# Kernel tuning notes

Measured on AMD Instinct MI355X. Metric: run time of the kernel, lower is better.

## Reference

```python
import jax, jax.numpy as jnp
import numpy as np

B, S, D = 2, 2048, 2048
H, KV, HD = 32, 8, 64
REP = H // KV


def rotate_half(t):
    t1, t2 = t[..., : t.shape[-1] // 2], t[..., t.shape[-1] // 2 :]
    return jnp.concatenate((-t2, t1), axis=-1)


def setup_inputs() -> dict:
    key = jax.random.key(0)
    kx, kq, kk, kv, ko = jax.random.split(key, 5)
    x = jax.random.normal(kx, (B, S, D), dtype=jnp.float32) * 0.02
    # RoPE tables: shape [S, HD//2]; forward concatenates [cos, cos] to reach HD
    inv_freq = 1.0 / (10000.0 ** (np.arange(0, HD, 2, dtype=np.float32) / HD))
    freqs = np.outer(np.arange(S, dtype=np.float32), inv_freq)
    cos = jnp.asarray(np.cos(freqs), dtype=jnp.float32)
    sin = jnp.asarray(np.sin(freqs), dtype=jnp.float32)
    # causal additive mask [1,1,S,S]
    causal = np.tril(np.ones((S, S), dtype=bool))
    mask = jnp.asarray(np.where(causal, 0.0, -1e9).astype(np.float32))[None, None]
    s = 0.02
    wq = jax.random.normal(kq, (H * HD, D), dtype=jnp.float32) * s
    wk = jax.random.normal(kk, (KV * HD, D), dtype=jnp.float32) * s
    wv = jax.random.normal(kv, (KV * HD, D), dtype=jnp.float32) * s
    wo = jax.random.normal(ko, (D, H * HD), dtype=jnp.float32) * s
    return {"x": x, "cos": cos, "sin": sin, "mask": mask,
            "wq": wq, "wk": wk, "wv": wv, "wo": wo}


def reference(x, cos, sin, mask, wq, wk, wv, wo):
    b, s, d = x.shape
    # QKV projections (Linear with bias=False: x @ W^T)
    q = jnp.einsum("bsd,ed->bse", x, wq).reshape(b, s, H, HD)
    k = jnp.einsum("bsd,ed->bse", x, wk).reshape(b, s, KV, HD)
    v = jnp.einsum("bsd,ed->bse", x, wv).reshape(b, s, KV, HD)
    # RoPE: cos/sin [S, HD//2] -> [1, S, 1, HD]
    cc = jnp.concatenate([cos[:s], cos[:s]], axis=-1)[None, :, None, :]
    ss = jnp.concatenate([sin[:s], sin[:s]], axis=-1)[None, :, None, :]
    q = q * cc + rotate_half(q) * ss
    k = k * cc + rotate_half(k) * ss
    # GQA: group q heads by kv head (implicit broadcast instead of repeat_kv)
    q = q.transpose(0, 2, 1, 3).reshape(b, KV, REP, s, HD)  # [B,KV,REP,S,HD]
    k = k.transpose(0, 2, 1, 3)                              # [B,KV,S,HD]
    v = v.transpose(0, 2, 1, 3)                              # [B,KV,S,HD]
    scores = jnp.einsum("bkrqd,bksd->bkrqs", q, k) / np.sqrt(HD)
    scores = scores + mask[:, :, None, :, :]  # broadcast over rep dim
    probs = jax.nn.softmax(scores.astype(jnp.float32), axis=-1).astype(q.dtype)
    out = jnp.einsum("bkrqs,bksd->bkrqd", probs, v)
    out = out.transpose(0, 3, 1, 2, 4).reshape(b, s, H * HD)  # [B,S,H*HD]
    return jnp.einsum("bse,de->bsd", out, wo)
```

## Files before the change

### kernel.cpp

```cpp
#include <hip/hip_runtime.h>
#include <stdint.h>

#define DEV __device__ __forceinline__

typedef __bf16 bf16;
typedef __bf16 bf16x8 __attribute__((ext_vector_type(8)));
typedef __bf16 bf16x4v __attribute__((ext_vector_type(4)));
typedef float f32x4 __attribute__((ext_vector_type(4)));
typedef float f32x16 __attribute__((ext_vector_type(16)));
typedef int int2v __attribute__((ext_vector_type(2)));

constexpr int Bb = 2, Ss = 2048, Dd = 2048, Hh = 32, KVh = 8, HDd = 64;
constexpr int Mm = Bb * Ss;
constexpr int EQ = Hh * HDd;
constexpr int EKV = KVh * HDd;
constexpr int Ee = EQ + 2 * EKV;

DEV void gload16(const void* g, void* l) {
  __builtin_amdgcn_global_load_lds((const __attribute__((address_space(1))) uint32_t*)g,
                                   (__attribute__((address_space(3))) uint32_t*)l, 16, 0, 0);
}

DEV float exp2_fast(float x) {
  float r;
  asm("v_exp_f32 %0, %1\n\ts_nop 0" : "=v"(r) : "v"(x));
  return r;
}
DEV uint32_t cvtpk(float lo, float hi) {
  uint32_t w;
  asm("v_cvt_pk_bf16_f32 %0, %1, %2" : "=v"(w) : "v"(lo), "v"(hi));
  return w;
}
DEV int2v pswap(uint32_t a, uint32_t b) {
  return __builtin_amdgcn_permlane32_swap((int)a, (int)b, false, false);
}
DEV float fu(uint32_t u) { union { uint32_t u; float f; } c; c.u = u; return c.f; }
DEV uint32_t uf(float f) { union { float f; uint32_t u; } c; c.f = f; return c.u; }

__global__ void cvt_kernel(const float* __restrict__ x, const float* __restrict__ wq,
                           const float* __restrict__ wk, const float* __restrict__ wv,
                           const float* __restrict__ wo,
                           bf16* __restrict__ xb, bf16* __restrict__ wqkvb,
                           bf16* __restrict__ wob) {
  const long NX = (long)Mm * Dd;
  const long NQ = (long)EQ * Dd;
  const long NK = (long)EKV * Dd;
  const long NO = (long)Dd * EQ;
  const long total4 = (NX + NQ + 2 * NK + NO) / 4;
  for (long i = (long)blockIdx.x * blockDim.x + threadIdx.x; i < total4;
       i += (long)gridDim.x * blockDim.x) {
    long e = i * 4;
    const float* src; bf16* dst;
    if (e < NX)                { src = x + e;                       dst = xb + e; }
    else if (e < NX + NQ)      { long o = e - NX;                   src = wq + o; dst = wqkvb + o; }
    else if (e < NX + NQ + NK) { long o = e - NX - NQ;              src = wk + o; dst = wqkvb + NQ + o; }
    else if (e < NX + NQ + 2*NK){ long o = e - NX - NQ - NK;        src = wv + o; dst = wqkvb + NQ + NK + o; }
    else                       { long o = e - NX - NQ - 2*NK;       src = wo + o; dst = wob + o; }
    float4 v = *(const float4*)src;
    bf16x4v b;
    b.x = (bf16)v.x; b.y = (bf16)v.y; b.z = (bf16)v.z; b.w = (bf16)v.w;
    *(bf16x4v*)dst = b;
  }
}

template <int BN, bool OUT_BF16>
__global__ __launch_bounds__(512, 1)
void gemm_bt(const bf16* __restrict__ A, const bf16* __restrict__ Bt,
             float* __restrict__ Cf, bf16* __restrict__ Cb,
             int Mn, int Nn, int Kn) {
  constexpr int NJ = BN / 64;
  constexpr int RB = BN / 4;
  __shared__ __align__(16) bf16 As[2][256 * 64];
  __shared__ __align__(16) bf16 Bs[2][BN * 64];
  const int tid = threadIdx.x, wid = tid >> 6, lane = tid & 63;
  const int g = lane >> 4, c = lane & 15;
  const int wm = wid >> 2, wn = wid & 3;

  const int nbj = Nn / BN;
  const int nwg = (Mn >> 8) * nbj;
  const int cpx = nwg >> 3;
  const int swz = ((int)blockIdx.x % 8) * cpx + (int)blockIdx.x / 8;
  const int bi = swz / nbj, bj = swz % nbj;
  const long arow0 = (long)bi * 256, brow0 = (long)bj * BN;

  const int srow = tid >> 3, schk = tid & 7;
  const int cs = schk ^ (srow & 7);

  f32x4 acc[8][NJ] = {};

#pragma unroll
  for (int it = 0; it < 4; ++it)
    gload16(A + (arow0 + it * 64 + srow) * Kn + cs * 8,
            (char*)&As[0][0] + it * 8192 + tid * 16);
#pragma unroll
  for (int q = 0; q < NJ; ++q)
    gload16(Bt + (brow0 + q * 64 + srow) * Kn + cs * 8,
            (char*)&Bs[0][0] + q * 8192 + tid * 16);
  __syncthreads();

  const int NT = Kn >> 6;
  for (int kt = 0; kt < NT; ++kt) {
    const char* pa = (const char*)&As[kt & 1][0];
    const char* pb = (const char*)&Bs[kt & 1][0];
    char* na = (char*)&As[(kt + 1) & 1][0];
    char* nb = (char*)&Bs[(kt + 1) & 1][0];
    const bool more = (kt + 1 < NT);
    bf16x8 bfr[NJ][2];

#pragma unroll
    for (int p = 0; p < 4; ++p) {
      bf16x8 af[2][2];
#pragma unroll
      for (int i2 = 0; i2 < 2; ++i2)
#pragma unroll
        for (int ks = 0; ks < 2; ++ks) {
          int r = wm * 128 + (2 * p + i2) * 16 + c;
          af[i2][ks] = *(const bf16x8*)(pa + r * 128 + (((ks * 4 + g) ^ (r & 7)) << 4));
        }
      if (p == 0) {
#pragma unroll
        for (int j = 0; j < NJ; ++j)
#pragma unroll
          for (int ks = 0; ks < 2; ++ks) {
            int r = wn * RB + j * 16 + c;
            bfr[j][ks] = *(const bf16x8*)(pb + r * 128 + (((ks * 4 + g) ^ (r & 7)) << 4));
          }
      }
      if (more) {
        if (p < NJ)
          gload16(Bt + (brow0 + p * 64 + srow) * Kn + (kt + 1) * 64 + cs * 8,
                  nb + p * 8192 + tid * 16);
        gload16(A + (arow0 + p * 64 + srow) * Kn + (kt + 1) * 64 + cs * 8,
                na + p * 8192 + tid * 16);
      }
      __builtin_amdgcn_s_barrier();
      asm volatile("s_waitcnt lgkmcnt(0)" ::: "memory");
      __builtin_amdgcn_s_setprio(1);
#pragma unroll
      for (int i2 = 0; i2 < 2; ++i2)
#pragma unroll
        for (int j = 0; j < NJ; ++j)
#pragma unroll
          for (int ks = 0; ks < 2; ++ks)
            acc[2 * p + i2][j] =
                __builtin_amdgcn_mfma_f32_16x16x32_bf16(af[i2][ks], bfr[j][ks],
                                                        acc[2 * p + i2][j], 0, 0, 0);
      __builtin_amdgcn_s_setprio(0);
      if (p == 1) asm volatile("s_waitcnt vmcnt(4)" ::: "memory");
      if (p < 3) __builtin_amdgcn_s_barrier();
    }
    asm volatile("s_waitcnt vmcnt(1)" ::: "memory");
    __builtin_amdgcn_s_barrier();
  }

#pragma unroll
  for (int i = 0; i < 8; ++i)
#pragma unroll
    for (int j = 0; j < NJ; ++j)
#pragma unroll
      for (int r = 0; r < 4; ++r) {
        long row = arow0 + wm * 128 + i * 16 + 4 * g + r;
        long col = brow0 + wn * RB + j * 16 + c;
        if (OUT_BF16) Cb[row * Nn + col] = (bf16)acc[i][j][r];
        else          Cf[row * Nn + col] = acc[i][j][r];
      }
}

__global__ void kv_prep_kernel(const bf16* __restrict__ qkv, const float* __restrict__ cosT,
                               const float* __restrict__ sinT, bf16* __restrict__ kout,
                               bf16* __restrict__ vtb) {
  if (blockIdx.x < 512) {
    __shared__ __align__(16) unsigned short tile[64][72];
    int blk = blockIdx.x;
    int st = blk & 31, kvh = (blk >> 5) & 7, b = blk >> 8;
    int s0 = st * 64;
    int t = threadIdx.x;
#pragma unroll
    for (int rep = 0; rep < 2; ++rep) {
      int idx = t + rep * 256;
      int r = idx >> 3, cb = idx & 7;
      const bf16* src = qkv + ((long)(b * Ss + s0 + r)) * Ee + EQ + EKV + kvh * 64 + cb * 8;
      *(uint4*)&tile[r][cb * 8] = *(const uint4*)src;
    }
    __syncthreads();
#pragma unroll
    for (int rep = 0; rep < 2; ++rep) {
      int idx = t + rep * 256;
      int dd = idx >> 3, scb = idx & 7;
      union { unsigned short u[8]; uint4 v; } pk;
#pragma unroll
      for (int j = 0; j < 8; ++j) pk.u[j] = tile[scb * 8 + j][dd];
      long dst = ((long)((b * KVh + kvh) * 64 + dd)) * Ss + s0 + scb * 8;
      *(uint4*)&vtb[dst] = pk.v;
    }
  } else {
    int tid = (int)(blockIdx.x - 512) * blockDim.x + threadIdx.x;
    int d = tid & 31;
    int h = (tid >> 5) & (KVh - 1);
    int m = tid >> 8;
    if (m >= Mm) return;
    int s = m & (Ss - 1), b = m >> 11;
    float lo = (float)qkv[(long)m * Ee + EQ + h * 64 + d];
    float hi = (float)qkv[(long)m * Ee + EQ + h * 64 + d + 32];
    float cs = cosT[s * 32 + d], sn = sinT[s * 32 + d];
    long base = (((long)(b * KVh + h)) * Ss + s) * 64;
    kout[base + d]      = (bf16)(lo * cs - hi * sn);
    kout[base + d + 32] = (bf16)(hi * cs + lo * sn);
  }
}

__global__ __launch_bounds__(512)
void attn_kernel(const bf16* __restrict__ qkv, const float* __restrict__ cosT,
                 const float* __restrict__ sinT, const bf16* __restrict__ k,
                 const bf16* __restrict__ vt, bf16* __restrict__ o) {
  __shared__ __align__(16) bf16 Kt[2][2][64 * 64];
  __shared__ __align__(16) bf16 Vt[2][2][64 * 64];
  constexpr float SCL = 0.18033688f;

  const int tid = threadIdx.x, qw = tid >> 6, lane = tid & 63;
  const int ql = lane & 31, hi = lane >> 5;
  const int g6 = (int)(blockIdx.x >> 6);
  const int qt = (g6 < 4) ? (7 - g6) : (g6 - 4);
  const int bh = blockIdx.x & 63;
  const int b = bh >> 5, h = bh & 31;
  const int kvh = h >> 2;
  const int q0 = qt * 256;
  const int qw_q0 = q0 + qw * 32;

  const bf16* kbase = k + ((long)(b * KVh + kvh)) * Ss * 64;
  const bf16* vbase = vt + ((long)(b * KVh + kvh)) * 64 * Ss;

  const int srow = tid >> 3, scb = tid & 7;
  const int scbs = scb ^ (srow & 7);
  const int sdst = tid * 16;

  bf16x8 qf[4];
  {
    const int s_row = q0 + qw * 32 + ql;
    const bf16* qrow = qkv + ((long)(b * Ss + s_row)) * Ee + h * 64 + 8 * hi;
    bf16x8 qraw[4];
#pragma unroll
    for (int ks = 0; ks < 4; ++ks) qraw[ks] = *(const bf16x8*)(qrow + 16 * ks);
    float cs8[2][8], sn8[2][8];
#pragma unroll
    for (int ks2 = 0; ks2 < 2; ++ks2) {
      const float* cp = cosT + s_row * 32 + 16 * ks2 + 8 * hi;
      const float* sp = sinT + s_row * 32 + 16 * ks2 + 8 * hi;
      *(float4*)&cs8[ks2][0] = *(const float4*)cp;
      *(float4*)&cs8[ks2][4] = *(const float4*)(cp + 4);
      *(float4*)&sn8[ks2][0] = *(const float4*)sp;
      *(float4*)&sn8[ks2][4] = *(const float4*)(sp + 4);
    }
#pragma unroll
    for (int ks2 = 0; ks2 < 2; ++ks2)
#pragma unroll
      for (int j = 0; j < 8; ++j) {
        float lo = (float)qraw[ks2][j], hv = (float)qraw[ks2 + 2][j];
        qf[ks2][j]     = (bf16)((lo * cs8[ks2][j] - hv * sn8[ks2][j]) * SCL);
        qf[ks2 + 2][j] = (bf16)((hv * cs8[ks2][j] + lo * sn8[ks2][j]) * SCL);
      }
  }

  gload16(kbase + (long)srow * 64 + scbs * 8, (char*)&Kt[0][0][0] + sdst);
  gload16(kbase + ((long)64 + srow) * 64 + scbs * 8, (char*)&Kt[0][1][0] + sdst);
  gload16(vbase + (long)srow * Ss + scbs * 8, (char*)&Vt[0][0][0] + sdst);
  gload16(vbase + (long)srow * Ss + 64 + scbs * 8, (char*)&Vt[0][1][0] + sdst);
  __syncthreads();

  f32x16 Oacc0 = {}, Oacc1 = {};
  float l_run = 0.f;
  const int qa = qw_q0 + ql;
  const int nt = 4 * qt + 4;
  const int ntp = nt >> 1;
  const int tdiag = qw_q0 >> 6;

  int cur = 0;
  for (int pp = 0; pp < ntp; ++pp) {
    if (pp + 1 < ntp) {
      int nb = cur ^ 1;
      long t0 = (long)(2 * pp + 2) * 64;
      gload16(kbase + (t0 + srow) * 64 + scbs * 8, (char*)&Kt[nb][0][0] + sdst);
      gload16(kbase + (t0 + 64 + srow) * 64 + scbs * 8, (char*)&Kt[nb][1][0] + sdst);
      gload16(vbase + (long)srow * Ss + t0 + scbs * 8, (char*)&Vt[nb][0][0] + sdst);
      gload16(vbase + (long)srow * Ss + t0 + 64 + scbs * 8, (char*)&Vt[nb][1][0] + sdst);
    }

#pragma unroll
    for (int half = 0; half < 2; ++half) {
      const int t = 2 * pp + half;
      if (64 * t < qw_q0 + 32) {
        f32x16 s0 = {}, s1 = {};
        const char* kt = (const char*)&Kt[cur][half][0];
#pragma unroll
        for (int ks = 0; ks < 4; ++ks) {
          int chk = ((2 * ks + hi) ^ (ql & 7)) << 4;
          bf16x8 kf0 = *(const bf16x8*)(kt + ql * 128 + chk);
          bf16x8 kf1 = *(const bf16x8*)(kt + (32 + ql) * 128 + chk);
          s0 = __builtin_amdgcn_mfma_f32_32x32x16_bf16(kf0, qf[ks], s0, 0, 0, 0);
          s1 = __builtin_amdgcn_mfma_f32_32x32x16_bf16(kf1, qf[ks], s1, 0, 0, 0);
        }

        if (t == tdiag) {
#pragma unroll
          for (int r = 0; r < 16; ++r) {
            int kv0 = t * 64 + (r & 3) + 8 * (r >> 2) + 4 * hi;
            if (kv0 > qa)      s0[r] = -1e30f;
            if (kv0 + 32 > qa) s1[r] = -1e30f;
          }
        }

#pragma unroll
        for (int r = 0; r < 16; ++r) {
          s0[r] = exp2_fast(s0[r]);
          s1[r] = exp2_fast(s1[r]);
        }
        float sm[16];
#pragma unroll
        for (int r = 0; r < 16; ++r) sm[r] = s0[r] + s1[r];
#pragma unroll
        for (int st2 = 8; st2 > 0; st2 >>= 1)
#pragma unroll
          for (int r = 0; r < 8; ++r)
            if (r < st2) sm[r] += sm[r + st2];
        {
          int2v rr = pswap(uf(sm[0]), uf(sm[0]));
          l_run += fu(rr.x) + fu(rr.y);
        }

        const char* vtb0 = (const char*)&Vt[cur][half][0];
#pragma unroll
        for (int ks = 0; ks < 4; ++ks) {
          uint32_t pk01, pk23, pk45, pk67;
          if (ks < 2) {
            const int rb = (ks & 1) * 8;
            pk01 = cvtpk(s0[rb + 0], s0[rb + 1]);
            pk23 = cvtpk(s0[rb + 2], s0[rb + 3]);
            pk45 = cvtpk(s0[rb + 4], s0[rb + 5]);
            pk67 = cvtpk(s0[rb + 6], s0[rb + 7]);
          } else {
            const int rb = (ks & 1) * 8;
            pk01 = cvtpk(s1[rb + 0], s1[rb + 1]);
            pk23 = cvtpk(s1[rb + 2], s1[rb + 3]);
            pk45 = cvtpk(s1[rb + 4], s1[rb + 5]);
            pk67 = cvtpk(s1[rb + 6], s1[rb + 7]);
          }
          int2v w02 = pswap(pk01, pk45);
          int2v w13 = pswap(pk23, pk67);
          union { uint32_t u[4]; bf16x8 v; } pa;
          pa.u[0] = (uint32_t)w02.x; pa.u[1] = (uint32_t)w13.x;
          pa.u[2] = (uint32_t)w02.y; pa.u[3] = (uint32_t)w13.y;

          int chk = ((2 * ks + hi) ^ (ql & 7)) << 4;
          bf16x8 vf0 = *(const bf16x8*)(vtb0 + ql * 128 + chk);
          bf16x8 vf1 = *(const bf16x8*)(vtb0 + (32 + ql) * 128 + chk);
          Oacc0 = __builtin_amdgcn_mfma_f32_32x32x16_bf16(pa.v, vf0, Oacc0, 0, 0, 0);
          Oacc1 = __builtin_amdgcn_mfma_f32_32x32x16_bf16(pa.v, vf1, Oacc1, 0, 0, 0);
        }
      }
    }

    __syncthreads();
    cur ^= 1;
  }

  float linv = 1.0f / l_run;
#pragma unroll
  for (int r = 0; r < 16; ++r) {
    int qrow = (r & 3) + 8 * (r >> 2) + 4 * hi;
    float li = __shfl(linv, qrow);
    long orow = (long)b * Ss + q0 + 32 * qw + qrow;
    o[orow * EQ + h * 64 + ql]      = (bf16)(Oacc0[r] * li);
    o[orow * EQ + h * 64 + 32 + ql] = (bf16)(Oacc1[r] * li);
  }
}

extern "C" void kernel_launch(void* const* d_in, const int* in_sizes, int n_in,
                              void* d_out, int out_size, void* d_ws, size_t ws_size,
                              hipStream_t stream) {
  const float* x    = (const float*)d_in[0];
  const float* cosT = (const float*)d_in[1];
  const float* sinT = (const float*)d_in[2];
  const float* wq   = (const float*)d_in[4];
  const float* wk   = (const float*)d_in[5];
  const float* wv   = (const float*)d_in[6];
  const float* wo   = (const float*)d_in[7];

  if (ws_size < 104857600u) return;

  char* ws = (char*)d_ws;
  bf16* xb    = (bf16*)(ws + 0);
  bf16* wqkvb = (bf16*)(ws + 16777216);
  bf16* wob   = (bf16*)(ws + 29360128);
  bf16* qkvb  = (bf16*)(ws + 37748736);
  bf16* kb    = (bf16*)(ws + 79691776);
  bf16* vtb   = (bf16*)(ws + 83886080);
  bf16* attnb = (bf16*)(ws + 88080384);
  float* outp = (float*)d_out;

  cvt_kernel<<<dim3(2048), dim3(256), 0, stream>>>(x, wq, wk, wv, wo, xb, wqkvb, wob);
  gemm_bt<192, true><<<dim3((Mm / 256) * (Ee / 192)), dim3(512), 0, stream>>>(
      xb, wqkvb, (float*)nullptr, qkvb, Mm, Ee, Dd);
  kv_prep_kernel<<<dim3(512 + (Mm * KVh * 32) / 256), dim3(256), 0, stream>>>(
      qkvb, cosT, sinT, kb, vtb);
  attn_kernel<<<dim3(512), dim3(512), 0, stream>>>(qkvb, cosT, sinT, kb, vtb, attnb);
  gemm_bt<128, false><<<dim3((Mm / 256) * (EQ / 128)), dim3(512), 0, stream>>>(
      attnb, wob, outp, (bf16*)nullptr, Mm, EQ, EQ);
}
```

Before: 162.5 us.

## Deepen GEMM global-to-LDS prefetch to triple buffering

The bf16 GEMM moves from double to triple buffering in LDS. B tiles are now prefetched two k-steps ahead, and for BN=128 the A tiles are too. The vmcnt waits are retuned so more loads stay in flight, which should hide global memory latency behind the MFMA work. The cost is more LDS per block and waits that are hand-tuned per BN. If a count is wrong there is a race, or the loads end up serialized.

```diff
diff --git a/kernel.cpp b/kernel.cpp
--- a/kernel.cpp
+++ b/kernel.cpp
@@ -70,8 +70,10 @@
              int Mn, int Nn, int Kn) {
   constexpr int NJ = BN / 64;
   constexpr int RB = BN / 4;
-  __shared__ __align__(16) bf16 As[2][256 * 64];
-  __shared__ __align__(16) bf16 Bs[2][BN * 64];
+  constexpr int ABUF = (BN == 128) ? 3 : 2;
+  constexpr int AAHEAD = ABUF - 1;
+  __shared__ __align__(16) bf16 As[ABUF][256 * 64];
+  __shared__ __align__(16) bf16 Bs[3][BN * 64];
   const int tid = threadIdx.x, wid = tid >> 6, lane = tid & 63;
   const int g = lane >> 4, c = lane & 15;
   const int wm = wid >> 2, wn = wid & 3;
@@ -88,23 +90,28 @@
 
   f32x4 acc[8][NJ] = {};
 
-#pragma unroll
-  for (int it = 0; it < 4; ++it)
-    gload16(A + (arow0 + it * 64 + srow) * Kn + cs * 8,
-            (char*)&As[0][0] + it * 8192 + tid * 16);
-#pragma unroll
-  for (int q = 0; q < NJ; ++q)
-    gload16(Bt + (brow0 + q * 64 + srow) * Kn + cs * 8,
-            (char*)&Bs[0][0] + q * 8192 + tid * 16);
+  const int NT = Kn >> 6;
+#pragma unroll
+  for (int t0 = 0; t0 < AAHEAD; ++t0)
+#pragma unroll
+    for (int it = 0; it < 4; ++it)
+      gload16(A + (arow0 + it * 64 + srow) * Kn + t0 * 64 + cs * 8,
+              (char*)&As[t0][0] + it * 8192 + tid * 16);
+#pragma unroll
+  for (int t0 = 0; t0 < 2; ++t0)
+#pragma unroll
+    for (int q = 0; q < NJ; ++q)
+      gload16(Bt + (brow0 + q * 64 + srow) * Kn + t0 * 64 + cs * 8,
+              (char*)&Bs[t0][0] + q * 8192 + tid * 16);
   __syncthreads();
 
-  const int NT = Kn >> 6;
   for (int kt = 0; kt < NT; ++kt) {
-    const char* pa = (const char*)&As[kt & 1][0];
-    const char* pb = (const char*)&Bs[kt & 1][0];
-    char* na = (char*)&As[(kt + 1) & 1][0];
-    char* nb = (char*)&Bs[(kt + 1) & 1][0];
-    const bool more = (kt + 1 < NT);
+    const char* pa = (const char*)&As[kt % ABUF][0];
+    const char* pb = (const char*)&Bs[kt % 3][0];
+    char* na = (char*)&As[(kt + AAHEAD) % ABUF][0];
+    char* nb = (char*)&Bs[(kt + 2) % 3][0];
+    const bool moreA = (kt + AAHEAD < NT);
+    const bool moreB = (kt + 2 < NT);
     bf16x8 bfr[NJ][2];
 
 #pragma unroll
@@ -126,13 +133,12 @@
             bfr[j][ks] = *(const bf16x8*)(pb + r * 128 + (((ks * 4 + g) ^ (r & 7)) << 4));
           }
       }
-      if (more) {
-        if (p < NJ)
-          gload16(Bt + (brow0 + p * 64 + srow) * Kn + (kt + 1) * 64 + cs * 8,
-                  nb + p * 8192 + tid * 16);
-        gload16(A + (arow0 + p * 64 + srow) * Kn + (kt + 1) * 64 + cs * 8,
+      if (moreA)
+        gload16(A + (arow0 + p * 64 + srow) * Kn + (kt + AAHEAD) * 64 + cs * 8,
                 na + p * 8192 + tid * 16);
-      }
+      if (moreB && p < NJ)
+        gload16(Bt + (brow0 + p * 64 + srow) * Kn + (kt + 2) * 64 + cs * 8,
+                nb + p * 8192 + tid * 16);
       __builtin_amdgcn_s_barrier();
       asm volatile("s_waitcnt lgkmcnt(0)" ::: "memory");
       __builtin_amdgcn_s_setprio(1);
@@ -146,10 +152,12 @@
                 __builtin_amdgcn_mfma_f32_16x16x32_bf16(af[i2][ks], bfr[j][ks],
                                                         acc[2 * p + i2][j], 0, 0, 0);
       __builtin_amdgcn_s_setprio(0);
-      if (p == 1) asm volatile("s_waitcnt vmcnt(4)" ::: "memory");
+      if (BN == 192 && p == 1)
+        asm volatile("s_waitcnt vmcnt(4)" ::: "memory");
       if (p < 3) __builtin_amdgcn_s_barrier();
     }
-    asm volatile("s_waitcnt vmcnt(1)" ::: "memory");
+    if (BN == 192) asm volatile("s_waitcnt vmcnt(2)" ::: "memory");
+    else           asm volatile("s_waitcnt vmcnt(6)" ::: "memory");
     __builtin_amdgcn_s_barrier();
   }
 
```

Measured after the change: 167.2 us. +2.9%, slower.
